# Kernel tuning notes

Measured on AMD Instinct MI355X. Metric: run time of the kernel, lower is better.

Reference implementation:

```python
import jax, jax.numpy as jnp
import numpy as np

G = 64          # grid_size
BC = 16         # base_channels
LATENT = 128

def _conv3d_s2(x, w, b):
    # x: [B,C,D,H,W], w: [O,I,3,3,3], stride 2, pad 1
    y = jax.lax.conv_general_dilated(
        x, w, window_strides=(2, 2, 2), padding=((1, 1), (1, 1), (1, 1)),
        dimension_numbers=('NCDHW', 'OIDHW', 'NCDHW'))
    return y + b[None, :, None, None, None]

def setup_inputs() -> dict:
    key = jax.random.key(0)
    ks = jax.random.split(key, 9)
    B, N = 32, 16384
    partial_coords = jax.random.uniform(ks[0], (B, N, 3), jnp.float32, -1.0, 1.0)
    def he(k, shape, fan_in):
        return jax.random.normal(k, shape, jnp.float32) * np.float32(np.sqrt(2.0 / fan_in))
    w1 = he(ks[1], (BC, 1, 3, 3, 3), 1 * 27)
    b1 = jnp.zeros((BC,), jnp.float32)
    w2 = he(ks[2], (2 * BC, BC, 3, 3, 3), BC * 27)
    b2 = jnp.zeros((2 * BC,), jnp.float32)
    w3 = he(ks[3], (4 * BC, 2 * BC, 3, 3, 3), 2 * BC * 27)
    b3 = jnp.zeros((4 * BC,), jnp.float32)
    fc_in = 4 * BC * (G // 8) ** 3
    fc_w = he(ks[4], (LATENT, fc_in), fc_in)
    fc_b = jnp.zeros((LATENT,), jnp.float32)
    return {'partial_coords': partial_coords, 'w1': w1, 'b1': b1, 'w2': w2,
            'b2': b2, 'w3': w3, 'b3': b3, 'fc_w': fc_w, 'fc_b': fc_b}

def reference(partial_coords, w1, b1, w2, b2, w3, b3, fc_w, fc_b):
    B, N, _ = partial_coords.shape
    # voxelize: scale [-1,1] -> [0, G-1], truncate (matches torch .long()), clamp
    coords_scaled = (partial_coords + 1.0) * 0.5 * (G - 1)
    ci = jnp.clip(coords_scaled.astype(jnp.int32), 0, G - 1)  # [B,N,3] = (x,y,z)
    bidx = jnp.broadcast_to(jnp.arange(B, dtype=jnp.int32)[:, None], (B, N))
    grid = jnp.zeros((B, G, G, G), jnp.float32)
    # grid[b, z, y, x] = 1.0  (single vectorized scatter)
    grid = grid.at[bidx, ci[..., 2], ci[..., 1], ci[..., 0]].set(1.0)
    x = grid[:, None]  # [B,1,G,G,G]
    x = jax.nn.relu(_conv3d_s2(x, w1, b1))
    x = jax.nn.relu(_conv3d_s2(x, w2, b2))
    x = jax.nn.relu(_conv3d_s2(x, w3, b3))  # [B,4*BC,G/8,G/8,G/8]
    feat = x.reshape(B, -1)
    return feat @ fc_w.T + fc_b  # [B,128]
```

## Files before the change

### kernel.cpp

```cpp
#include <hip/hip_runtime.h>
#include <hip/hip_bf16.h>


typedef __attribute__((ext_vector_type(8))) short bf16x8;
typedef __attribute__((ext_vector_type(4))) float f32x4;

__device__ inline unsigned short f2bf(float f) {
    __hip_bfloat16 h = __float2bfloat16(f);
    return *reinterpret_cast<unsigned short*>(&h);
}

__global__ void k_scatter_wtrans(const float* __restrict__ coords,
                                 unsigned char* __restrict__ grid,
                                 const float* __restrict__ w2,
                                 unsigned short* __restrict__ w2b,
                                 const float* __restrict__ w3,
                                 unsigned short* __restrict__ w3b,
                                 const float* __restrict__ fc_w,
                                 unsigned short* __restrict__ fc_wb) {
    int blk = blockIdx.x;
    if (blk < 2048) {
        int i = blk * 256 + threadIdx.x;
        float cx = coords[3 * i + 0];
        float cy = coords[3 * i + 1];
        float cz = coords[3 * i + 2];
        int ix = (int)((cx + 1.0f) * 0.5f * 63.0f);
        int iy = (int)((cy + 1.0f) * 0.5f * 63.0f);
        int iz = (int)((cz + 1.0f) * 0.5f * 63.0f);
        ix = min(max(ix, 0), 63);
        iy = min(max(iy, 0), 63);
        iz = min(max(iz, 0), 63);
        int b = i >> 14;
        grid[((b * 64 + iz) * 64 + iy) * 64 + ix] = 1;
    } else if (blk < 2320) {
        int i = (blk - 2048) * 256 + threadIdx.x;
        if (i < 14336) {
            int sh = i >> 9, oc = (i >> 4) & 31, c = i & 15;
            float v = (sh < 27) ? w2[oc * 432 + c * 27 + sh] : 0.0f;
            w2b[i] = f2bf(v);
        } else {
            int j = i - 14336;
            if (j < 55296) {
                int sh = j >> 11, oc = (j >> 5) & 63, c = j & 31;
                w3b[j] = f2bf(w3[oc * 864 + c * 27 + sh]);
            }
        }
    } else {
        int u = (blk - 2320) * 256 + threadIdx.x;
        const float* src = fc_w + (size_t)u * 8;
        float4 lo = *(const float4*)src;
        float4 hi = *(const float4*)(src + 4);
        unsigned int dw[4];
        dw[0] = (unsigned int)f2bf(lo.x) | ((unsigned int)f2bf(lo.y) << 16);
        dw[1] = (unsigned int)f2bf(lo.z) | ((unsigned int)f2bf(lo.w) << 16);
        dw[2] = (unsigned int)f2bf(hi.x) | ((unsigned int)f2bf(hi.y) << 16);
        dw[3] = (unsigned int)f2bf(hi.z) | ((unsigned int)f2bf(hi.w) << 16);
        *(int4*)(fc_wb + (size_t)u * 8) = int4{(int)dw[0], (int)dw[1], (int)dw[2], (int)dw[3]};
    }
}

__global__ __launch_bounds__(256) void k_conv1(
        const unsigned char* __restrict__ grid,
        const float* __restrict__ w1,
        const float* __restrict__ b1,
        unsigned short* __restrict__ c1b) {
    __shared__ float hal[9 * 17 * 20];
    const int t = threadIdx.x;
    const int blk = blockIdx.x;
    const int b = blk >> 7;
    const int zb = (blk >> 4) & 7;
    const int yb = (blk >> 2) & 3;
    const int xb = blk & 3;
    const int iz0 = 8 * zb - 1, iy0 = 16 * yb - 1, ix0 = 16 * xb - 1;

    const unsigned char* g = grid + b * 262144;
    for (int i = t; i < 2601; i += 256) {
        int hz = i / 289, rm = i - hz * 289;
        int hy = rm / 17, hx = rm - hy * 17;
        int iz = iz0 + hz, iy = iy0 + hy, ix = ix0 + hx;
        bool ok = (iz >= 0) & (iy >= 0) & (ix >= 0);
        float v = ok ? (float)g[(iz * 64 + iy) * 64 + ix] : 0.0f;
        int ux = (hx & 1) ? 10 + (hx >> 1) : (hx >> 1);
        hal[(hz * 17 + hy) * 20 + ux] = v;
    }
    __syncthreads();

    const int x = t & 7, y = (t >> 3) & 7, tz = t >> 6;
    const int base = (2 * tz * 17) * 20 + (2 * y) * 20 + x;
    float in27[27];
#pragma unroll
    for (int kz = 0; kz < 3; ++kz)
#pragma unroll
        for (int ky = 0; ky < 3; ++ky)
#pragma unroll
            for (int kx = 0; kx < 3; ++kx) {
                int uxo = (kx == 1) ? 10 : ((kx == 2) ? 1 : 0);
                in27[kz * 9 + ky * 3 + kx] =
                    hal[base + (kz * 17 + ky) * 20 + uxo];
            }
    float r[16];
#pragma unroll
    for (int oc = 0; oc < 16; ++oc) {
        float acc = b1[oc];
#pragma unroll
        for (int k = 0; k < 27; ++k) acc = fmaf(w1[oc * 27 + k], in27[k], acc);
        r[oc] = fmaxf(acc, 0.0f);
    }
    unsigned int dw[8];
#pragma unroll
    for (int j = 0; j < 8; ++j)
        dw[j] = (unsigned int)f2bf(r[2 * j]) | ((unsigned int)f2bf(r[2 * j + 1]) << 16);
    int oz = 4 * zb + tz, oy = 8 * yb + y, ox = 8 * xb + x;
    size_t idx = ((size_t)(b * 32 + oz) * 32 + oy) * 32 + ox;
    char* base_o = (char*)c1b + idx * 32;
    *(int4*)base_o        = int4{(int)dw[0], (int)dw[1], (int)dw[2], (int)dw[3]};
    *(int4*)(base_o + 16) = int4{(int)dw[4], (int)dw[5], (int)dw[6], (int)dw[7]};
}

__device__ constexpr int abase2(int sh) {
    return (sh / 9) * 18480 + (((sh % 9) / 3) & 1) * 9520 +
           (((sh % 9) / 3) >> 1) * 560 + (sh % 3) * 32;
}

__global__ __launch_bounds__(512, 4) void k_conv2_mfma(
        const unsigned short* __restrict__ c1b,
        const unsigned short* __restrict__ w2b,
        const float* __restrict__ b2,
        unsigned short* __restrict__ c2b) {
    __shared__ __align__(16) char smem[55440];
    const int t = threadIdx.x;
    const int b = blockIdx.x >> 5;
    const int zo = (blockIdx.x >> 1) & 15;
    const int xh = blockIdx.x & 1;
    const int lane = t & 63;
    const int wid = t >> 6;

    const char* src = (const char*)c1b + (size_t)b * (32768 * 32);
    for (int i = t; i < 1683; i += 512) {
        int kz = i / 561, rem = i - kz * 561;
        int iy_st = rem / 17, c = rem - iy_st * 17;
        int iz = 2 * zo + kz - 1;
        int iy = iy_st - 1;
        int ix = (xh << 4) + c - 1;
        int4 v0 = {0, 0, 0, 0}, v1 = {0, 0, 0, 0};
        if ((iz >= 0) & (iy >= 0) & (ix >= 0)) {
            const char* gp = src + ((size_t)((iz * 32 + iy) * 32 + ix)) * 32;
            v0 = *(const int4*)gp;
            v1 = *(const int4*)(gp + 16);
        }
        char* d = smem + kz * 18480 + (iy_st & 1) * 9520 + (iy_st >> 1) * 560 + c * 32;
        *(int4*)d = v0;
        *(int4*)(d + 16) = v1;
    }
    __syncthreads();

    const int y16 = lane & 15;
    const int g = lane >> 4;
    const int h = g & 1;
    const int s = g >> 1;
    const int laneA = y16 * 560 + h * 16;
    const int laneB = (lane & 15) * 32 + h * 16 + s * 1024;
    const int xl64 = wid * 64;
    const char* wbase = (const char*)w2b;

    f32x4 acc0 = {0, 0, 0, 0}, acc1 = {0, 0, 0, 0};

#pragma unroll
    for (int sp = 0; sp < 14; ++sp) {
        const int sh0 = 2 * sp;
        const int sh1 = (2 * sp + 1 < 27) ? 2 * sp + 1 : 26;
        const int a0 = abase2(sh0);
        const int d01 = abase2(sh1) - a0;
        bf16x8 A = *(const bf16x8*)(smem + laneA + a0 + (s ? d01 : 0) + xl64);
        const char* wb = wbase + sp * 2048 + laneB;
        bf16x8 B0 = *(const bf16x8*)wb;
        bf16x8 B1 = *(const bf16x8*)(wb + 512);
        acc0 = __builtin_amdgcn_mfma_f32_16x16x32_bf16(A, B0, acc0, 0, 0, 0);
        acc1 = __builtin_amdgcn_mfma_f32_16x16x32_bf16(A, B1, acc1, 0, 0, 0);
    }

    __syncthreads();
    float* sOut = (float*)smem;
    {
        int ocl = lane & 15;
        int yb = (lane >> 4) * 4;
#pragma unroll
        for (int r = 0; r < 4; ++r) {
            sOut[ocl * 129        + (yb + r) * 8 + wid] = acc0[r];
            sOut[(ocl + 16) * 129 + (yb + r) * 8 + wid] = acc1[r];
        }
    }
    __syncthreads();
    {
        int vox = t >> 2, q = t & 3;
        unsigned int dw[4];
#pragma unroll
        for (int j = 0; j < 4; ++j) {
            int oc0 = 8 * q + 2 * j;
            float v0 = fmaxf(sOut[oc0 * 129 + vox] + b2[oc0], 0.0f);
            float v1 = fmaxf(sOut[(oc0 + 1) * 129 + vox] + b2[oc0 + 1], 0.0f);
            dw[j] = (unsigned int)f2bf(v0) | ((unsigned int)f2bf(v1) << 16);
        }
        char* dst = (char*)c2b +
                    ((size_t)b * 4096 + zo * 256 + (vox >> 3) * 16 + xh * 8 + (vox & 7)) * 64 +
                    q * 16;
        *(int4*)dst = int4{(int)dw[0], (int)dw[1], (int)dw[2], (int)dw[3]};
    }
}

__global__ __launch_bounds__(512) void k_conv3_mfma(
        const unsigned short* __restrict__ c2b,
        const unsigned short* __restrict__ w3b,
        const float* __restrict__ b3,
        unsigned short* __restrict__ featb) {
    __shared__ __align__(16) char smem[55488];
    const int t = threadIdx.x;
    const int b = blockIdx.x >> 3;
    const int zo = blockIdx.x & 7;
    const int lane = t & 63;
    const int wid = t >> 6;

    if (t < 396) {
        int p3 = t / 132, j = t % 132;
        int v = j >> 2, g = j & 3;
        int iy_st = (v < 17) ? 0 : (v - 16);
        int ix_st = (v < 17) ? v : 0;
        int ux = (ix_st & 1) ? 9 + (ix_st >> 1) : (ix_st >> 1);
        int u = (p3 * 17 + iy_st) * 17 + ux;
        *(int4*)(smem + u * 64 + g * 16) = int4{0, 0, 0, 0};
    }

    const char* src = (const char*)c2b + (size_t)b * 262144;
#pragma unroll
    for (int r = 0; r < 6; ++r) {
        int i = r * 512 + t;
        int g = i & 3, vox = i >> 2;
        int kz = vox >> 8, pos = vox & 255;
        int iy = pos >> 4, ix = pos & 15;
        int iz = 2 * zo + kz - 1;
        int4 v = {0, 0, 0, 0};
        if (iz >= 0)
            v = *(const int4*)(src + ((size_t)(iz * 256 + pos)) * 64 + g * 16);
        int ix_st = ix + 1;
        int ux = (ix_st & 1) ? 9 + (ix_st >> 1) : (ix_st >> 1);
        int u = (kz * 17 + iy + 1) * 17 + ux;
        *(int4*)(smem + u * 64 + g * 16) = v;
    }
    __syncthreads();

    const int mt = wid >> 1;
    const int ntp = wid & 1;
    const int m = mt * 16 + (lane & 15);
    const int y = m >> 3, x = m & 7;
    const int g = lane >> 4;
    const int laneA = (34 * y + x) * 64 + g * 16;
    const char* wb_base = (const char*)w3b + (ntp * 32 + (lane & 15)) * 64 + g * 16;

    f32x4 acc0 = {0, 0, 0, 0}, acc1 = {0, 0, 0, 0};

#pragma unroll
    for (int sh = 0; sh < 27; ++sh) {
        const int kz = sh / 9, ky = (sh % 9) / 3, kx = sh % 3;
        const int uxc = (kx == 0) ? 0 : ((kx == 1) ? 9 : 1);
        const int aoff = (289 * kz + 17 * ky + uxc) * 64;
        bf16x8 A = *(const bf16x8*)(smem + laneA + aoff);
        const char* wb = wb_base + sh * 4096;
        bf16x8 B0 = *(const bf16x8*)wb;
        bf16x8 B1 = *(const bf16x8*)(wb + 1024);
        acc0 = __builtin_amdgcn_mfma_f32_16x16x32_bf16(A, B0, acc0, 0, 0, 0);
        acc1 = __builtin_amdgcn_mfma_f32_16x16x32_bf16(A, B1, acc1, 0, 0, 0);
    }

    __syncthreads();
    float* sOut = (float*)smem;
    {
        int ocl = lane & 15;
        int mb = mt * 16 + (lane >> 4) * 4;
#pragma unroll
        for (int r = 0; r < 4; ++r) {
            sOut[(ntp * 32 + ocl) * 65 + mb + r]      = acc0[r];
            sOut[(ntp * 32 + 16 + ocl) * 65 + mb + r] = acc1[r];
        }
    }
    __syncthreads();
    {
        int oc = t >> 3, q = t & 7;
        float bb = b3[oc];
        unsigned int dw[4];
#pragma unroll
        for (int j = 0; j < 4; ++j) {
            float v0 = fmaxf(sOut[oc * 65 + q * 8 + 2 * j] + bb, 0.0f);
            float v1 = fmaxf(sOut[oc * 65 + q * 8 + 2 * j + 1] + bb, 0.0f);
            dw[j] = (unsigned int)f2bf(v0) | ((unsigned int)f2bf(v1) << 16);
        }
        char* dst = (char*)featb + (size_t)b * 65536 + oc * 1024 + zo * 128 + q * 16;
        *(int4*)dst = int4{(int)dw[0], (int)dw[1], (int)dw[2], (int)dw[3]};
    }
}

__global__ __launch_bounds__(256) void k_fc_mfma(
        const unsigned short* __restrict__ featb,
        const unsigned short* __restrict__ fc_wb,
        const float* __restrict__ fc_b,
        float* __restrict__ out) {
    __shared__ __align__(16) char smem[32 * 272];
    const int t = threadIdx.x;
    const int blk = blockIdx.x;
    const int f0 = blk << 7;

    {
        int b = t >> 3, seg = t & 7;
        const char* gp = (const char*)featb + (size_t)b * 65536 + f0 * 2 + seg * 32;
        char* d = smem + b * 272 + seg * 32;
        *(int4*)d = *(const int4*)gp;
        *(int4*)(d + 16) = *(const int4*)(gp + 16);
    }
    __syncthreads();

    const int lane = t & 63;
    const int w = t >> 6;
    const int n = lane & 15;
    const int g = lane >> 4;

    f32x4 acc00 = {0, 0, 0, 0}, acc01 = {0, 0, 0, 0};
    f32x4 acc10 = {0, 0, 0, 0}, acc11 = {0, 0, 0, 0};

    const char* wb0 = (const char*)fc_wb + ((size_t)(2 * w * 16 + n)) * 65536 + f0 * 2 + g * 16;
    const char* wb1 = wb0 + 16 * 65536;

#pragma unroll
    for (int ks = 0; ks < 4; ++ks) {
        bf16x8 A0 = *(const bf16x8*)(smem + n * 272 + ks * 64 + g * 16);
        bf16x8 A1 = *(const bf16x8*)(smem + (16 + n) * 272 + ks * 64 + g * 16);
        bf16x8 B0 = *(const bf16x8*)(wb0 + ks * 64);
        bf16x8 B1 = *(const bf16x8*)(wb1 + ks * 64);
        acc00 = __builtin_amdgcn_mfma_f32_16x16x32_bf16(A0, B0, acc00, 0, 0, 0);
        acc10 = __builtin_amdgcn_mfma_f32_16x16x32_bf16(A1, B0, acc10, 0, 0, 0);
        acc01 = __builtin_amdgcn_mfma_f32_16x16x32_bf16(A0, B1, acc01, 0, 0, 0);
        acc11 = __builtin_amdgcn_mfma_f32_16x16x32_bf16(A1, B1, acc11, 0, 0, 0);
    }

    const int bo = (lane >> 4) * 4;
    const int l0 = 2 * w * 16 + (lane & 15);
    const int l1 = l0 + 16;
    const bool bias = (blk == 0);
    const float bb0 = bias ? fc_b[l0] : 0.0f;
    const float bb1 = bias ? fc_b[l1] : 0.0f;
#pragma unroll
    for (int r = 0; r < 4; ++r) {
        atomicAdd(&out[(bo + r) * 128 + l0],      acc00[r] + bb0);
        atomicAdd(&out[(bo + r + 16) * 128 + l0], acc10[r] + bb0);
        atomicAdd(&out[(bo + r) * 128 + l1],      acc01[r] + bb1);
        atomicAdd(&out[(bo + r + 16) * 128 + l1], acc11[r] + bb1);
    }
}

extern "C" void kernel_launch(void* const* d_in, const int* in_sizes, int n_in,
                              void* d_out, int out_size, void* d_ws, size_t ws_size,
                              hipStream_t stream) {
    const float* coords = (const float*)d_in[0];
    const float* w1 = (const float*)d_in[1];
    const float* b1 = (const float*)d_in[2];
    const float* w2 = (const float*)d_in[3];
    const float* b2 = (const float*)d_in[4];
    const float* w3 = (const float*)d_in[5];
    const float* b3 = (const float*)d_in[6];
    const float* fc_w = (const float*)d_in[7];
    const float* fc_b = (const float*)d_in[8];

    unsigned char* grid_u8 = (unsigned char*)d_ws;
    unsigned short* c1b = (unsigned short*)((char*)d_ws + 8388608);
    unsigned short* c2b = (unsigned short*)((char*)d_ws + 75497472);
    unsigned short* featb = (unsigned short*)((char*)d_ws + 92274688);
    unsigned short* w2b = (unsigned short*)((char*)d_ws + 98566144);
    unsigned short* w3b = (unsigned short*)((char*)d_ws + 98697216);
    unsigned short* fc_wb = (unsigned short*)((char*)d_ws + 98807808);
    float* out = (float*)d_out;

    hipMemsetAsync(grid_u8, 0, 8388608, stream);
    hipMemsetAsync(out, 0, 32 * 128 * sizeof(float), stream);

    k_scatter_wtrans<<<4368, 256, 0, stream>>>(coords, grid_u8, w2, w2b, w3, w3b,
                                               fc_w, fc_wb);
    k_conv1<<<4096, 256, 0, stream>>>(grid_u8, w1, b1, c1b);
    k_conv2_mfma<<<1024, 512, 0, stream>>>(c1b, w2b, b2, c2b);
    k_conv3_mfma<<<256, 512, 0, stream>>>(c2b, w3b, b3, featb);
    k_fc_mfma<<<256, 256, 0, stream>>>(featb, fc_wb, fc_b, out);
}
```

Baseline: 159.8 us.

## Fuse conv1 into conv2 kernel, computing conv1 halo on the fly

Removes the separate conv1 kernel and its 64MB bf16 intermediate tensor. Each conv2 block now loads a u8 occupancy-grid slab into shared memory and computes the conv1 outputs for its input halo directly into the conv2 shared tile. This trades global memory traffic and a kernel launch for some redundant conv1 compute on overlapping halos, plus extra shared memory that may lower occupancy.

```diff
diff --git a/kernel.cpp b/kernel.cpp
--- a/kernel.cpp
+++ b/kernel.cpp
@@ -59,74 +59,19 @@
     }
 }
 
-__global__ __launch_bounds__(256) void k_conv1(
+__device__ constexpr int abase2(int sh) {
+    return (sh / 9) * 18480 + (((sh % 9) / 3) & 1) * 9520 +
+           (((sh % 9) / 3) >> 1) * 560 + (sh % 3) * 32;
+}
+
+__global__ __launch_bounds__(512, 4) void k_conv12_mfma(
         const unsigned char* __restrict__ grid,
         const float* __restrict__ w1,
         const float* __restrict__ b1,
-        unsigned short* __restrict__ c1b) {
-    __shared__ float hal[9 * 17 * 20];
-    const int t = threadIdx.x;
-    const int blk = blockIdx.x;
-    const int b = blk >> 7;
-    const int zb = (blk >> 4) & 7;
-    const int yb = (blk >> 2) & 3;
-    const int xb = blk & 3;
-    const int iz0 = 8 * zb - 1, iy0 = 16 * yb - 1, ix0 = 16 * xb - 1;
-
-    const unsigned char* g = grid + b * 262144;
-    for (int i = t; i < 2601; i += 256) {
-        int hz = i / 289, rm = i - hz * 289;
-        int hy = rm / 17, hx = rm - hy * 17;
-        int iz = iz0 + hz, iy = iy0 + hy, ix = ix0 + hx;
-        bool ok = (iz >= 0) & (iy >= 0) & (ix >= 0);
-        float v = ok ? (float)g[(iz * 64 + iy) * 64 + ix] : 0.0f;
-        int ux = (hx & 1) ? 10 + (hx >> 1) : (hx >> 1);
-        hal[(hz * 17 + hy) * 20 + ux] = v;
-    }
-    __syncthreads();
-
-    const int x = t & 7, y = (t >> 3) & 7, tz = t >> 6;
-    const int base = (2 * tz * 17) * 20 + (2 * y) * 20 + x;
-    float in27[27];
-#pragma unroll
-    for (int kz = 0; kz < 3; ++kz)
-#pragma unroll
-        for (int ky = 0; ky < 3; ++ky)
-#pragma unroll
-            for (int kx = 0; kx < 3; ++kx) {
-                int uxo = (kx == 1) ? 10 : ((kx == 2) ? 1 : 0);
-                in27[kz * 9 + ky * 3 + kx] =
-                    hal[base + (kz * 17 + ky) * 20 + uxo];
-            }
-    float r[16];
-#pragma unroll
-    for (int oc = 0; oc < 16; ++oc) {
-        float acc = b1[oc];
-#pragma unroll
-        for (int k = 0; k < 27; ++k) acc = fmaf(w1[oc * 27 + k], in27[k], acc);
-        r[oc] = fmaxf(acc, 0.0f);
-    }
-    unsigned int dw[8];
-#pragma unroll
-    for (int j = 0; j < 8; ++j)
-        dw[j] = (unsigned int)f2bf(r[2 * j]) | ((unsigned int)f2bf(r[2 * j + 1]) << 16);
-    int oz = 4 * zb + tz, oy = 8 * yb + y, ox = 8 * xb + x;
-    size_t idx = ((size_t)(b * 32 + oz) * 32 + oy) * 32 + ox;
-    char* base_o = (char*)c1b + idx * 32;
-    *(int4*)base_o        = int4{(int)dw[0], (int)dw[1], (int)dw[2], (int)dw[3]};
-    *(int4*)(base_o + 16) = int4{(int)dw[4], (int)dw[5], (int)dw[6], (int)dw[7]};
-}
-
-__device__ constexpr int abase2(int sh) {
-    return (sh / 9) * 18480 + (((sh % 9) / 3) & 1) * 9520 +
-           (((sh % 9) / 3) >> 1) * 560 + (sh % 3) * 32;
-}
-
-__global__ __launch_bounds__(512, 4) void k_conv2_mfma(
-        const unsigned short* __restrict__ c1b,
         const unsigned short* __restrict__ w2b,
         const float* __restrict__ b2,
         unsigned short* __restrict__ c2b) {
+    __shared__ __align__(16) unsigned int gslab[4224];
     __shared__ __align__(16) char smem[55440];
     const int t = threadIdx.x;
     const int b = blockIdx.x >> 5;
@@ -135,22 +80,61 @@
     const int lane = t & 63;
     const int wid = t >> 6;
 
-    const char* src = (const char*)c1b + (size_t)b * (32768 * 32);
-    for (int i = t; i < 1683; i += 512) {
-        int kz = i / 561, rem = i - kz * 561;
-        int iy_st = rem / 17, c = rem - iy_st * 17;
-        int iz = 2 * zo + kz - 1;
-        int iy = iy_st - 1;
-        int ix = (xh << 4) + c - 1;
-        int4 v0 = {0, 0, 0, 0}, v1 = {0, 0, 0, 0};
-        if ((iz >= 0) & (iy >= 0) & (ix >= 0)) {
-            const char* gp = src + ((size_t)((iz * 32 + iy) * 32 + ix)) * 32;
-            v0 = *(const int4*)gp;
-            v1 = *(const int4*)(gp + 16);
-        }
-        char* d = smem + kz * 18480 + (iy_st & 1) * 9520 + (iy_st >> 1) * 560 + c * 32;
-        *(int4*)d = v0;
-        *(int4*)(d + 16) = v1;
+    {
+        const unsigned char* gb = grid + b * 262144;
+        const int gz0 = 4 * zo - 3;
+        for (int i = t; i < 4221; i += 512) {
+            int gz = i / 603, rem = i - gz * 603;
+            int gy = rem / 9, d = rem - gy * 9;
+            int z = gz0 + gz, y = gy - 3, x4 = 32 * xh - 4 + 4 * d;
+            unsigned int v = 0;
+            if ((z >= 0) & (y >= 0) & (x4 >= 0))
+                v = *(const unsigned int*)(gb + (z * 64 + y) * 64 + x4);
+            gslab[i] = v;
+        }
+    }
+    __syncthreads();
+
+    {
+        const unsigned char* gs = (const unsigned char*)gslab;
+        for (int i = t; i < 1683; i += 512) {
+            int kz = i / 561, rem = i - kz * 561;
+            int iy_st = rem / 17, c = rem - iy_st * 17;
+            char* dstp = smem + kz * 18480 + (iy_st & 1) * 9520 +
+                         (iy_st >> 1) * 560 + c * 32;
+            int iz = 2 * zo + kz - 1, iy = iy_st - 1, ix = 16 * xh + c - 1;
+            if ((iz | iy | ix) < 0) {
+                *(int4*)dstp = int4{0, 0, 0, 0};
+                *(int4*)(dstp + 16) = int4{0, 0, 0, 0};
+                continue;
+            }
+            float acc[16];
+#pragma unroll
+            for (int ch = 0; ch < 16; ++ch) acc[ch] = b1[ch];
+            const int sz0 = 2 * kz, sy0 = 2 * iy_st, sx0 = 2 * c + 1;
+#pragma unroll
+            for (int kz2 = 0; kz2 < 3; ++kz2)
+#pragma unroll
+                for (int ky2 = 0; ky2 < 3; ++ky2)
+#pragma unroll
+                    for (int kx2 = 0; kx2 < 3; ++kx2) {
+                        float fg = (float)gs[((sz0 + kz2) * 67 + sy0 + ky2) * 36 +
+                                             sx0 + kx2];
+                        const int t27 = kz2 * 9 + ky2 * 3 + kx2;
+#pragma unroll
+                        for (int ch = 0; ch < 16; ++ch)
+                            acc[ch] = fmaf(w1[ch * 27 + t27], fg, acc[ch]);
+                    }
+            unsigned int dw[8];
+#pragma unroll
+            for (int j = 0; j < 8; ++j) {
+                unsigned short lo = f2bf(fmaxf(acc[2 * j], 0.0f));
+                unsigned short hi = f2bf(fmaxf(acc[2 * j + 1], 0.0f));
+                dw[j] = (unsigned int)lo | ((unsigned int)hi << 16);
+            }
+            *(int4*)dstp = int4{(int)dw[0], (int)dw[1], (int)dw[2], (int)dw[3]};
+            *(int4*)(dstp + 16) = int4{(int)dw[4], (int)dw[5], (int)dw[6], (int)dw[7]};
+        }
     }
     __syncthreads();
 
@@ -369,7 +353,6 @@
     const float* fc_b = (const float*)d_in[8];
 
     unsigned char* grid_u8 = (unsigned char*)d_ws;
-    unsigned short* c1b = (unsigned short*)((char*)d_ws + 8388608);
     unsigned short* c2b = (unsigned short*)((char*)d_ws + 75497472);
     unsigned short* featb = (unsigned short*)((char*)d_ws + 92274688);
     unsigned short* w2b = (unsigned short*)((char*)d_ws + 98566144);
@@ -382,8 +365,7 @@
 
     k_scatter_wtrans<<<4368, 256, 0, stream>>>(coords, grid_u8, w2, w2b, w3, w3b,
                                                fc_w, fc_wb);
-    k_conv1<<<4096, 256, 0, stream>>>(grid_u8, w1, b1, c1b);
-    k_conv2_mfma<<<1024, 512, 0, stream>>>(c1b, w2b, b2, c2b);
+    k_conv12_mfma<<<1024, 512, 0, stream>>>(grid_u8, w1, b1, w2b, b2, c2b);
     k_conv3_mfma<<<256, 512, 0, stream>>>(c2b, w3b, b3, featb);
     k_fc_mfma<<<256, 256, 0, stream>>>(featb, fc_wb, fc_b, out);
 }
```

Result: no change. 159.9 us (+0.1%).
